# Kernel tuning notes

Hardware: AMD Instinct MI355X
Metric: run time of the kernel (lower is better)

Reference implementation:

```python
import jax, jax.numpy as jnp
import numpy as np
import math

D_MODEL = 1024
D_STATE = 64
DT_MIN = 0.001
DT_MAX = 0.1
BATCH = 4
SEQLEN = 4096


def make_hippo_matrix(N):
    P = np.sqrt(1 + 2 * np.arange(N))
    A = P[:, np.newaxis] * P[np.newaxis, :]
    A = np.tril(A) - np.diag(np.arange(N))
    return jnp.asarray(-A, dtype=jnp.float32)


def setup_inputs() -> dict:
    key = jax.random.key(0)
    k_u, k_B, k_C, k_D, k_dt = jax.random.split(key, 5)
    u = jax.random.normal(k_u, (BATCH, SEQLEN, D_MODEL), dtype=jnp.float32)
    A = make_hippo_matrix(D_STATE)  # (N, N) HiPPO-LegS buffer
    B = jax.random.normal(k_B, (D_STATE, 1), dtype=jnp.float32)
    C = jax.random.normal(k_C, (1, D_STATE), dtype=jnp.float32)
    D = jax.random.normal(k_D, (1,), dtype=jnp.float32)
    log_dt = (jax.random.uniform(k_dt, (1,), dtype=jnp.float32)
              * (math.log(DT_MAX) - math.log(DT_MIN)) + math.log(DT_MIN))
    return {"u": u, "A": A, "B": B, "C": C, "D": D, "log_dt": log_dt}


def _forward(u, A, B, C, D, log_dt):
    n = A.shape[0]
    dt = jnp.exp(log_dt)[0]
    A_bar = jax.scipy.linalg.expm(dt * A)                     # (N, N)
    B_bar = jnp.linalg.solve(A, (A_bar - jnp.eye(n, dtype=A.dtype)) @ B)  # (N, 1)
    bvec = B_bar[:, 0]          # (N,)
    cvec = C[0]                 # (N,)
    d_scalar = D[0]
    # Faithful to source: only channel 0 of u drives the SSM.
    u0 = u[:, :, 0]             # (Bn, L)

    def step(x, u_t):
        # x: (Bn, N), u_t: (Bn,)
        x = x @ A_bar.T + u_t[:, None] * bvec
        y = x @ cvec + d_scalar * u_t   # (Bn,)
        return x, y

    x0 = jnp.zeros((u.shape[0], n), dtype=u.dtype)
    _, ys = jax.lax.scan(step, x0, jnp.swapaxes(u0, 0, 1))   # (L, Bn)
    # Scalar output broadcast across all H channels (matches torch expand)
    y = jnp.broadcast_to(jnp.swapaxes(ys, 0, 1)[:, :, None], u.shape)
    return y


def reference(u, A, B, C, D, log_dt):
    return _forward(u, A, B, C, D, log_dt)
```

## Files before the change

kernel.cpp:

```cpp
#include <hip/hip_runtime.h>


#define NT 1024
#define MP 68
#define MSZ (64 * MP)
#define MOFF 4096
#define U0OFF (4096 + 8 * MSZ)

typedef __attribute__((ext_vector_type(8))) short v8s;
typedef __attribute__((ext_vector_type(4))) float v4f;

__device__ __forceinline__ unsigned short bf16r(float x) {
  union { float f; unsigned u; } v; v.f = x;
  unsigned r = v.u + 0x7fffu + ((v.u >> 16) & 1u);
  return (unsigned short)(r >> 16);
}
__device__ __forceinline__ float bf2f(unsigned short h) {
  union { unsigned u; float f; } v; v.u = ((unsigned)h) << 16;
  return v.f;
}

__device__ void mm_mfma(const float* gA, int aT, const float* gB, float* gC,
                        int pc, int nct, int colbase, unsigned short* FRAG) {
  const int t = threadIdx.x;
  __syncthreads();
  {
    const int slot = t >> 1;
    const int jh = (t & 1) * 4;
    const int l = slot & 63;
    const int Tq = slot >> 6;
    const int mrow = (Tq >> 1) * 16 + (l & 15);
    const int kk = (Tq & 1) * 32 + (l >> 4) * 8 + jh;
    float x0, x1, x2, x3;
    if (!aT) {
      const float4 f = *(const float4*)(gA + mrow * MP + kk);
      x0 = f.x; x1 = f.y; x2 = f.z; x3 = f.w;
    } else {
      x0 = gA[(kk + 0) * MP + mrow]; x1 = gA[(kk + 1) * MP + mrow];
      x2 = gA[(kk + 2) * MP + mrow]; x3 = gA[(kk + 3) * MP + mrow];
    }
    unsigned short h0 = bf16r(x0), h1 = bf16r(x1), h2 = bf16r(x2), h3 = bf16r(x3);
    ushort4 H, L;
    H.x = h0; H.y = h1; H.z = h2; H.w = h3;
    L.x = bf16r(x0 - bf2f(h0)); L.y = bf16r(x1 - bf2f(h1));
    L.z = bf16r(x2 - bf2f(h2)); L.w = bf16r(x3 - bf2f(h3));
    *(ushort4*)(FRAG + slot * 8 + jh) = H;
    *(ushort4*)(FRAG + 4096 + slot * 8 + jh) = L;
    const float y0 = gB[(kk + 0) * MP + mrow], y1 = gB[(kk + 1) * MP + mrow];
    const float y2 = gB[(kk + 2) * MP + mrow], y3 = gB[(kk + 3) * MP + mrow];
    unsigned short g0 = bf16r(y0), g1 = bf16r(y1), g2 = bf16r(y2), g3 = bf16r(y3);
    H.x = g0; H.y = g1; H.z = g2; H.w = g3;
    L.x = bf16r(y0 - bf2f(g0)); L.y = bf16r(y1 - bf2f(g1));
    L.z = bf16r(y2 - bf2f(g2)); L.w = bf16r(y3 - bf2f(g3));
    *(ushort4*)(FRAG + 8192 + slot * 8 + jh) = H;
    *(ushort4*)(FRAG + 12288 + slot * 8 + jh) = L;
  }
  __syncthreads();
  {
    const int w = t >> 6, l = t & 63;
    const int R = w >> 2, Cc = w & 3;
    if (Cc < nct) {
      const v8s Ah0 = *(const v8s*)(FRAG + ((R * 2 + 0) * 64 + l) * 8);
      const v8s Ah1 = *(const v8s*)(FRAG + ((R * 2 + 1) * 64 + l) * 8);
      const v8s Al0 = *(const v8s*)(FRAG + 4096 + ((R * 2 + 0) * 64 + l) * 8);
      const v8s Al1 = *(const v8s*)(FRAG + 4096 + ((R * 2 + 1) * 64 + l) * 8);
      const v8s Bh0 = *(const v8s*)(FRAG + 8192 + ((Cc * 2 + 0) * 64 + l) * 8);
      const v8s Bh1 = *(const v8s*)(FRAG + 8192 + ((Cc * 2 + 1) * 64 + l) * 8);
      const v8s Bl0 = *(const v8s*)(FRAG + 12288 + ((Cc * 2 + 0) * 64 + l) * 8);
      const v8s Bl1 = *(const v8s*)(FRAG + 12288 + ((Cc * 2 + 1) * 64 + l) * 8);
      v4f acc = {0.f, 0.f, 0.f, 0.f};
      acc = __builtin_amdgcn_mfma_f32_16x16x32_bf16(Ah0, Bh0, acc, 0, 0, 0);
      acc = __builtin_amdgcn_mfma_f32_16x16x32_bf16(Ah1, Bh1, acc, 0, 0, 0);
      acc = __builtin_amdgcn_mfma_f32_16x16x32_bf16(Ah0, Bl0, acc, 0, 0, 0);
      acc = __builtin_amdgcn_mfma_f32_16x16x32_bf16(Ah1, Bl1, acc, 0, 0, 0);
      acc = __builtin_amdgcn_mfma_f32_16x16x32_bf16(Al0, Bh0, acc, 0, 0, 0);
      acc = __builtin_amdgcn_mfma_f32_16x16x32_bf16(Al1, Bh1, acc, 0, 0, 0);
      const int col = colbase + Cc * 16 + (l & 15);
      const int r0 = R * 16 + (l >> 4) * 4;
      gC[(r0 + 0) * pc + col] = acc[0];
      gC[(r0 + 1) * pc + col] = acc[1];
      gC[(r0 + 2) * pc + col] = acc[2];
      gC[(r0 + 3) * pc + col] = acc[3];
    }
  }
  __syncthreads();
}

__device__ __forceinline__ void mv64(const float* Mm, const float* vin,
                                     float* vout, float* vscr) {
  __syncthreads();
  const int t = threadIdx.x, i = t & 63, c = t >> 6;
  const float4 m = *(const float4*)(Mm + i * MP + c * 4);
  vscr[t] = fmaf(m.x, vin[c * 4 + 0], fmaf(m.y, vin[c * 4 + 1],
            fmaf(m.z, vin[c * 4 + 2], m.w * vin[c * 4 + 3])));
  __syncthreads();
  if (t < 64) {
    float s = 0.f;
#pragma unroll
    for (int cc = 0; cc < 16; ++cc) s += vscr[cc * 64 + t];
    vout[t] = s;
  }
  __syncthreads();
}

__device__ void buildC(float* dst, const float* X, const float* X2, const float* X3,
                       float c0, float c1, float c2, float c3, int add) {
  __syncthreads();
  for (int e = threadIdx.x; e < 64 * MP; e += NT) {
    const int r = e / MP, c = e - r * MP;
    if (c < 64) {
      float v = c1 * X[e] + c2 * X2[e] + c3 * X3[e];
      if (c == r) v += c0;
      dst[e] = add ? dst[e] + v : v;
    }
  }
  __syncthreads();
}

__global__ __launch_bounds__(NT) void s4_setup(const float* __restrict__ u,
    const float* __restrict__ A, const float* __restrict__ Bv,
    const float* __restrict__ Cv, const float* __restrict__ logdt,
    float* __restrict__ ws) {
  if (blockIdx.x > 0) {
    const int idx = (blockIdx.x - 1) * NT + threadIdx.x;
    ws[U0OFF + idx] = u[(size_t)idx * 1024];
    return;
  }
  __shared__ __align__(16) unsigned short FRAG[16384];
  __shared__ float vscr[NT];
  __shared__ float va[64], vb[64], vg[64];
  __shared__ int s_s;
  float* Xc = (float*)FRAG;

  const int t = threadIdx.x;
  float* kbuf = ws;
  float* M0 = ws + MOFF;          float* M1 = M0 + MSZ;
  float* M2 = M1 + MSZ;           float* M3 = M2 + MSZ;
  float* M4 = M3 + MSZ;           float* M5 = M4 + MSZ;
  float* M6 = M5 + MSZ;           float* M7 = M6 + MSZ;
  const float dt = expf(logdt[0]);

  const float invf[17] = {1.f, 1.f, 1.f / 2.f, 1.f / 6.f, 1.f / 24.f, 1.f / 120.f,
                          1.f / 720.f, 1.f / 5040.f, 1.f / 40320.f, 1.f / 362880.f,
                          1.f / 3628800.f, 1.f / 39916800.f, 1.f / 479001600.f,
                          1.f / 6.2270208e9f, 1.f / 8.71782912e10f,
                          1.f / 1.307674368e12f, 1.f / 2.0922789888e13f};

  {
    const int j = t & 63, ch = t >> 6;
    float p = 0.f;
#pragma unroll
    for (int ii = 0; ii < 4; ++ii) p += fabsf(A[(ch * 4 + ii) * 64 + j]);
    vscr[t] = p;
    __syncthreads();
    if (t < 64) {
      float cs = 0.f;
#pragma unroll
      for (int c = 0; c < 16; ++c) cs += vscr[c * 64 + t];
      cs *= dt;
#pragma unroll
      for (int off = 32; off > 0; off >>= 1) cs = fmaxf(cs, __shfl_xor(cs, off));
      if (t == 0) {
        int s = 0;
        while (cs > 2.0f && s < 30) { cs *= 0.5f; ++s; }
        s_s = s;
      }
    }
    __syncthreads();
  }
  const int sq = s_s;
  const float scl = ldexpf(dt, -sq);

  {
    const float4 a4 = *(const float4*)(A + t * 4);
    float4 x;
    x.x = a4.x * scl; x.y = a4.y * scl; x.z = a4.z * scl; x.w = a4.w * scl;
    const int r = t >> 4, c4 = (t & 15) * 4;
    *(float4*)(M0 + r * MP + c4) = x;
    *(float4*)(Xc + r * MP + c4) = x;
  }
  __syncthreads();

  if (t < 64) { va[t] = Bv[t]; vg[t] = Bv[t]; }
  {
    float* vc = va; float* vn = vb;
    for (int k = 1; k <= 15; ++k) {
      mv64(Xc, vc, vn, vscr);
      if (t < 64) vg[t] = fmaf(vn[t], invf[k + 1], vg[t]);
      float* tmp = vc; vc = vn; vn = tmp;
    }
    __syncthreads();
  }

  mm_mfma(M0, 0, M0, M1, MP, 4, 0, FRAG);
  mm_mfma(M1, 0, M0, M2, MP, 4, 0, FRAG);
  mm_mfma(M1, 0, M1, M3, MP, 4, 0, FRAG);
  buildC(M5, M0, M1, M2, invf[12], invf[13], invf[14], invf[15], 0);
  mm_mfma(M5, 0, M3, M4, MP, 4, 0, FRAG);
  buildC(M4, M0, M1, M2, invf[8], invf[9], invf[10], invf[11], 1);
  mm_mfma(M4, 0, M3, M5, MP, 4, 0, FRAG);
  buildC(M5, M0, M1, M2, invf[4], invf[5], invf[6], invf[7], 1);
  mm_mfma(M5, 0, M3, M4, MP, 4, 0, FRAG);
  buildC(M4, M0, M1, M2, invf[0], invf[1], invf[2], invf[3], 1);

  float* F = M4; float* Fo = M5;
  for (int it = 0; it < sq; ++it) {
    mv64(F, vg, va, vscr);
    if (t < 64) vg[t] = 0.5f * (va[t] + vg[t]);
    mm_mfma(F, 0, F, Fo, MP, 4, 0, FRAG);
    float* tmp = F; F = Fo; Fo = tmp;
  }

  __syncthreads();
  {
    const int r = t >> 4, c4 = (t & 15) * 4;
    *(float4*)(Xc + r * MP + c4) = *(const float4*)(F + r * MP + c4);
  }
  if (t < 64) { va[t] = dt * vg[t]; M6[t * MP + 0] = dt * vg[t]; }
  __syncthreads();
  {
    float* vc = va; float* vn = vb;
    for (int r = 1; r < 16; ++r) {
      mv64(Xc, vc, vn, vscr);
      if (t < 64) M6[t * MP + r] = vn[t];
      float* tmp = vc; vc = vn; vn = tmp;
    }
    __syncthreads();
  }

  mm_mfma(F, 0, F, M0, MP, 4, 0, FRAG);
  mm_mfma(M0, 0, M0, M1, MP, 4, 0, FRAG);
  mm_mfma(M1, 0, M1, M0, MP, 4, 0, FRAG);
  mm_mfma(M0, 0, M0, M1, MP, 4, 0, FRAG);
  mm_mfma(M1, 0, M6, M6, MP, 1, 16, FRAG);
  mm_mfma(M1, 0, M1, M0, MP, 4, 0, FRAG);
  mm_mfma(M0, 0, M6, M6, MP, 2, 32, FRAG);
  mm_mfma(M0, 0, M0, M1, MP, 4, 0, FRAG);

  __syncthreads();
  for (int e = t; e < 4096; e += NT) {
    const int r = e >> 6, c = e & 63;
    Xc[c * MP + r] = M1[r * MP + c];
  }
  __syncthreads();
  if (t < 64) { va[t] = Cv[t]; M7[t * MP + 0] = Cv[t]; }
  __syncthreads();
  {
    float* vc = va; float* vn = vb;
    for (int q = 1; q < 16; ++q) {
      mv64(Xc, vc, vn, vscr);
      if (t < 64) M7[t * MP + q] = vn[t];
      float* tmp = vc; vc = vn; vn = tmp;
    }
    __syncthreads();
  }

  mm_mfma(M1, 0, M1, M0, MP, 4, 0, FRAG);
  mm_mfma(M0, 0, M0, M2, MP, 4, 0, FRAG);
  mm_mfma(M2, 0, M2, M0, MP, 4, 0, FRAG);
  mm_mfma(M0, 0, M0, M2, MP, 4, 0, FRAG);
  mm_mfma(M2, 1, M7, M7, MP, 1, 16, FRAG);
  mm_mfma(M2, 0, M2, M0, MP, 4, 0, FRAG);
  mm_mfma(M0, 1, M7, M7, MP, 2, 32, FRAG);

  mm_mfma(M7, 1, M6, kbuf, 64, 4, 0, FRAG);
}

__global__ __launch_bounds__(256) void s4_out(const float* __restrict__ ws,
                                              const float* __restrict__ Dp,
                                              float* __restrict__ out) {
  const int bid = blockIdx.x;
  const int b = bid >> 10;
  const int t0 = (bid & 1023) << 2;
  const float* kb = ws;
  const float* ub = ws + U0OFF + (b << 12);
  const int tid = threadIdx.x;
  const int t3 = t0 + 3;
  float a0 = 0.f, a1 = 0.f, a2 = 0.f, a3 = 0.f;
  for (int j = tid; j <= t3; j += 256) {
    const float kj = kb[j];
    if (j <= t0)     a0 = fmaf(kj, ub[t0 - j], a0);
    if (j <= t0 + 1) a1 = fmaf(kj, ub[t0 + 1 - j], a1);
    if (j <= t0 + 2) a2 = fmaf(kj, ub[t0 + 2 - j], a2);
    a3 = fmaf(kj, ub[t3 - j], a3);
  }
#pragma unroll
  for (int off = 32; off > 0; off >>= 1) {
    a0 += __shfl_xor(a0, off);
    a1 += __shfl_xor(a1, off);
    a2 += __shfl_xor(a2, off);
    a3 += __shfl_xor(a3, off);
  }
  __shared__ float red[4][4];
  __shared__ float sy[4];
  if ((tid & 63) == 0) {
    const int w = tid >> 6;
    red[0][w] = a0; red[1][w] = a1; red[2][w] = a2; red[3][w] = a3;
  }
  __syncthreads();
  if (tid < 4)
    sy[tid] = red[tid][0] + red[tid][1] + red[tid][2] + red[tid][3] +
              Dp[0] * ub[t0 + tid];
  __syncthreads();
  const int row = tid >> 6, l = tid & 63;
  const float y = sy[row];
  const float4 y4 = make_float4(y, y, y, y);
  float4* dst = (float4*)(out + ((size_t)(b << 12) + t0 + row) * 1024);
  dst[l] = y4; dst[l + 64] = y4; dst[l + 128] = y4; dst[l + 192] = y4;
}

extern "C" void kernel_launch(void* const* d_in, const int* in_sizes, int n_in,
                              void* d_out, int out_size, void* d_ws, size_t ws_size,
                              hipStream_t stream) {
  const float* u  = (const float*)d_in[0];
  const float* A  = (const float*)d_in[1];
  const float* B  = (const float*)d_in[2];
  const float* C  = (const float*)d_in[3];
  const float* D  = (const float*)d_in[4];
  const float* ld = (const float*)d_in[5];
  float* ws = (float*)d_ws;

  s4_setup<<<17, NT, 0, stream>>>(u, A, B, C, ld, ws);
  s4_out<<<4096, 256, 0, stream>>>(ws, D, (float*)d_out);
}
```

Measured before the change: 182.2 us.

## Keep running matrix power in LDS and restructure setup matrix chain

Restructures the single-block setup kernel so the running matrix (powers of A, expm result) lives in shared memory instead of global workspace. Matrix products are done in place through the fragment staging buffer, and the B-side Taylor series is evaluated with a Horner-style scheme on three precomputed powers. The Krylov/kernel blocks are stored transposed, so the final product needs no explicit transpose pass. The aim is to cut global-memory round trips and serial mat-vec steps in the latency-bound setup. The cost is heavier LDS use and in-place aliasing of the matrix operands.

```diff
diff --git a/kernel.cpp b/kernel.cpp
--- a/kernel.cpp
+++ b/kernel.cpp
@@ -3,9 +3,7 @@
 
 #define NT 1024
 #define MP 68
-#define MSZ (64 * MP)
-#define MOFF 4096
-#define U0OFF (4096 + 8 * MSZ)
+#define MB (64 * MP)
 
 typedef __attribute__((ext_vector_type(8))) short v8s;
 typedef __attribute__((ext_vector_type(4))) float v4f;
@@ -20,8 +18,10 @@
   return v.f;
 }
 
-__device__ void mm_mfma(const float* gA, int aT, const float* gB, float* gC,
-                        int pc, int nct, int colbase, unsigned short* FRAG) {
+__device__ void mm(const float* Ag, const float* Bs, int bT,
+                   float* Cd, int cpitch, float* Cd2,
+                   int nrt, int nct, int rowbase, int colbase,
+                   unsigned short* FRAG) {
   const int t = threadIdx.x;
   __syncthreads();
   {
@@ -31,66 +31,73 @@
     const int Tq = slot >> 6;
     const int mrow = (Tq >> 1) * 16 + (l & 15);
     const int kk = (Tq & 1) * 32 + (l >> 4) * 8 + jh;
-    float x0, x1, x2, x3;
-    if (!aT) {
-      const float4 f = *(const float4*)(gA + mrow * MP + kk);
-      x0 = f.x; x1 = f.y; x2 = f.z; x3 = f.w;
-    } else {
-      x0 = gA[(kk + 0) * MP + mrow]; x1 = gA[(kk + 1) * MP + mrow];
-      x2 = gA[(kk + 2) * MP + mrow]; x3 = gA[(kk + 3) * MP + mrow];
-    }
-    unsigned short h0 = bf16r(x0), h1 = bf16r(x1), h2 = bf16r(x2), h3 = bf16r(x3);
+    const float4 f = *(const float4*)(Ag + mrow * MP + kk);
     ushort4 H, L;
-    H.x = h0; H.y = h1; H.z = h2; H.w = h3;
-    L.x = bf16r(x0 - bf2f(h0)); L.y = bf16r(x1 - bf2f(h1));
-    L.z = bf16r(x2 - bf2f(h2)); L.w = bf16r(x3 - bf2f(h3));
+    unsigned short h;
+    h = bf16r(f.x); H.x = h; L.x = bf16r(f.x - bf2f(h));
+    h = bf16r(f.y); H.y = h; L.y = bf16r(f.y - bf2f(h));
+    h = bf16r(f.z); H.z = h; L.z = bf16r(f.z - bf2f(h));
+    h = bf16r(f.w); H.w = h; L.w = bf16r(f.w - bf2f(h));
     *(ushort4*)(FRAG + slot * 8 + jh) = H;
     *(ushort4*)(FRAG + 4096 + slot * 8 + jh) = L;
-    const float y0 = gB[(kk + 0) * MP + mrow], y1 = gB[(kk + 1) * MP + mrow];
-    const float y2 = gB[(kk + 2) * MP + mrow], y3 = gB[(kk + 3) * MP + mrow];
-    unsigned short g0 = bf16r(y0), g1 = bf16r(y1), g2 = bf16r(y2), g3 = bf16r(y3);
-    H.x = g0; H.y = g1; H.z = g2; H.w = g3;
-    L.x = bf16r(y0 - bf2f(g0)); L.y = bf16r(y1 - bf2f(g1));
-    L.z = bf16r(y2 - bf2f(g2)); L.w = bf16r(y3 - bf2f(g3));
+    float y0, y1, y2, y3;
+    if (bT) {
+      const float4 g = *(const float4*)(Bs + mrow * MP + kk);
+      y0 = g.x; y1 = g.y; y2 = g.z; y3 = g.w;
+    } else {
+      y0 = Bs[(kk + 0) * MP + mrow]; y1 = Bs[(kk + 1) * MP + mrow];
+      y2 = Bs[(kk + 2) * MP + mrow]; y3 = Bs[(kk + 3) * MP + mrow];
+    }
+    h = bf16r(y0); H.x = h; L.x = bf16r(y0 - bf2f(h));
+    h = bf16r(y1); H.y = h; L.y = bf16r(y1 - bf2f(h));
+    h = bf16r(y2); H.z = h; L.z = bf16r(y2 - bf2f(h));
+    h = bf16r(y3); H.w = h; L.w = bf16r(y3 - bf2f(h));
     *(ushort4*)(FRAG + 8192 + slot * 8 + jh) = H;
     *(ushort4*)(FRAG + 12288 + slot * 8 + jh) = L;
   }
   __syncthreads();
   {
     const int w = t >> 6, l = t & 63;
-    const int R = w >> 2, Cc = w & 3;
-    if (Cc < nct) {
-      const v8s Ah0 = *(const v8s*)(FRAG + ((R * 2 + 0) * 64 + l) * 8);
-      const v8s Ah1 = *(const v8s*)(FRAG + ((R * 2 + 1) * 64 + l) * 8);
-      const v8s Al0 = *(const v8s*)(FRAG + 4096 + ((R * 2 + 0) * 64 + l) * 8);
-      const v8s Al1 = *(const v8s*)(FRAG + 4096 + ((R * 2 + 1) * 64 + l) * 8);
-      const v8s Bh0 = *(const v8s*)(FRAG + 8192 + ((Cc * 2 + 0) * 64 + l) * 8);
-      const v8s Bh1 = *(const v8s*)(FRAG + 8192 + ((Cc * 2 + 1) * 64 + l) * 8);
-      const v8s Bl0 = *(const v8s*)(FRAG + 12288 + ((Cc * 2 + 0) * 64 + l) * 8);
-      const v8s Bl1 = *(const v8s*)(FRAG + 12288 + ((Cc * 2 + 1) * 64 + l) * 8);
-      v4f acc = {0.f, 0.f, 0.f, 0.f};
-      acc = __builtin_amdgcn_mfma_f32_16x16x32_bf16(Ah0, Bh0, acc, 0, 0, 0);
-      acc = __builtin_amdgcn_mfma_f32_16x16x32_bf16(Ah1, Bh1, acc, 0, 0, 0);
-      acc = __builtin_amdgcn_mfma_f32_16x16x32_bf16(Ah0, Bl0, acc, 0, 0, 0);
-      acc = __builtin_amdgcn_mfma_f32_16x16x32_bf16(Ah1, Bl1, acc, 0, 0, 0);
-      acc = __builtin_amdgcn_mfma_f32_16x16x32_bf16(Al0, Bh0, acc, 0, 0, 0);
-      acc = __builtin_amdgcn_mfma_f32_16x16x32_bf16(Al1, Bh1, acc, 0, 0, 0);
-      const int col = colbase + Cc * 16 + (l & 15);
-      const int r0 = R * 16 + (l >> 4) * 4;
-      gC[(r0 + 0) * pc + col] = acc[0];
-      gC[(r0 + 1) * pc + col] = acc[1];
-      gC[(r0 + 2) * pc + col] = acc[2];
-      gC[(r0 + 3) * pc + col] = acc[3];
-    }
-  }
-  __syncthreads();
-}
-
-__device__ __forceinline__ void mv64(const float* Mm, const float* vin,
-                                     float* vout, float* vscr) {
+    if (w < 4 && w < nrt) {
+      const v8s Ah0 = *(const v8s*)(FRAG + ((w * 2 + 0) * 64 + l) * 8);
+      const v8s Ah1 = *(const v8s*)(FRAG + ((w * 2 + 1) * 64 + l) * 8);
+      const v8s Al0 = *(const v8s*)(FRAG + 4096 + ((w * 2 + 0) * 64 + l) * 8);
+      const v8s Al1 = *(const v8s*)(FRAG + 4096 + ((w * 2 + 1) * 64 + l) * 8);
+      for (int Cc = 0; Cc < nct; ++Cc) {
+        const v8s Bh0 = *(const v8s*)(FRAG + 8192 + ((Cc * 2 + 0) * 64 + l) * 8);
+        const v8s Bh1 = *(const v8s*)(FRAG + 8192 + ((Cc * 2 + 1) * 64 + l) * 8);
+        const v8s Bl0 = *(const v8s*)(FRAG + 12288 + ((Cc * 2 + 0) * 64 + l) * 8);
+        const v8s Bl1 = *(const v8s*)(FRAG + 12288 + ((Cc * 2 + 1) * 64 + l) * 8);
+        v4f acc = {0.f, 0.f, 0.f, 0.f};
+        acc = __builtin_amdgcn_mfma_f32_16x16x32_bf16(Ah0, Bh0, acc, 0, 0, 0);
+        acc = __builtin_amdgcn_mfma_f32_16x16x32_bf16(Ah1, Bh1, acc, 0, 0, 0);
+        acc = __builtin_amdgcn_mfma_f32_16x16x32_bf16(Ah0, Bl0, acc, 0, 0, 0);
+        acc = __builtin_amdgcn_mfma_f32_16x16x32_bf16(Ah1, Bl1, acc, 0, 0, 0);
+        acc = __builtin_amdgcn_mfma_f32_16x16x32_bf16(Al0, Bh0, acc, 0, 0, 0);
+        acc = __builtin_amdgcn_mfma_f32_16x16x32_bf16(Al1, Bh1, acc, 0, 0, 0);
+        const int col = colbase + Cc * 16 + (l & 15);
+        const int r0 = rowbase + w * 16 + (l >> 4) * 4;
+        Cd[(r0 + 0) * cpitch + col] = acc[0];
+        Cd[(r0 + 1) * cpitch + col] = acc[1];
+        Cd[(r0 + 2) * cpitch + col] = acc[2];
+        Cd[(r0 + 3) * cpitch + col] = acc[3];
+        if (Cd2) {
+          Cd2[(r0 + 0) * MP + col] = acc[0];
+          Cd2[(r0 + 1) * MP + col] = acc[1];
+          Cd2[(r0 + 2) * MP + col] = acc[2];
+          Cd2[(r0 + 3) * MP + col] = acc[3];
+        }
+      }
+    }
+  }
+  __syncthreads();
+}
+
+__device__ __forceinline__ void mv64row(const float* M, const float* vin,
+                                        float* vout, float* vscr) {
   __syncthreads();
   const int t = threadIdx.x, i = t & 63, c = t >> 6;
-  const float4 m = *(const float4*)(Mm + i * MP + c * 4);
+  const float4 m = *(const float4*)(M + i * MP + c * 4);
   vscr[t] = fmaf(m.x, vin[c * 4 + 0], fmaf(m.y, vin[c * 4 + 1],
             fmaf(m.z, vin[c * 4 + 2], m.w * vin[c * 4 + 3])));
   __syncthreads();
@@ -103,15 +110,34 @@
   __syncthreads();
 }
 
-__device__ void buildC(float* dst, const float* X, const float* X2, const float* X3,
-                       float c0, float c1, float c2, float c3, int add) {
-  __syncthreads();
-  for (int e = threadIdx.x; e < 64 * MP; e += NT) {
+__device__ __forceinline__ void mv64colT(const float* M, const float* vin,
+                                         float* vout, float* vscr) {
+  __syncthreads();
+  const int t = threadIdx.x, i = t & 63, c = t >> 6;
+  float p = 0.f;
+#pragma unroll
+  for (int j = 0; j < 4; ++j) p = fmaf(M[(c * 4 + j) * MP + i], vin[c * 4 + j], p);
+  vscr[t] = p;
+  __syncthreads();
+  if (t < 64) {
+    float s = 0.f;
+#pragma unroll
+    for (int cc = 0; cc < 16; ++cc) s += vscr[cc * 64 + t];
+    vout[t] = s;
+  }
+  __syncthreads();
+}
+
+__device__ void buildG(float* dst, const float* X, const float* X2, const float* X3,
+                       float c0, float c1, float c2, float c3, const float* addsrc) {
+  __syncthreads();
+  for (int e = threadIdx.x; e < MB; e += NT) {
     const int r = e / MP, c = e - r * MP;
     if (c < 64) {
       float v = c1 * X[e] + c2 * X2[e] + c3 * X3[e];
-      if (c == r) v += c0;
-      dst[e] = add ? dst[e] + v : v;
+      if (r == c) v += c0;
+      if (addsrc) v += addsrc[e];
+      dst[e] = v;
     }
   }
   __syncthreads();
@@ -123,21 +149,24 @@
     float* __restrict__ ws) {
   if (blockIdx.x > 0) {
     const int idx = (blockIdx.x - 1) * NT + threadIdx.x;
-    ws[U0OFF + idx] = u[(size_t)idx * 1024];
+    ws[4096 + idx] = u[(size_t)idx * 1024];
     return;
   }
+  __shared__ __align__(16) float S0[MB];
   __shared__ __align__(16) unsigned short FRAG[16384];
-  __shared__ float vscr[NT];
-  __shared__ float va[64], vb[64], vg[64];
+  __shared__ float vB[64], v1[64], v2[64], v3[64], va[64], vb[64], vg[64];
   __shared__ int s_s;
-  float* Xc = (float*)FRAG;
+  float* vscr = (float*)FRAG;
 
   const int t = threadIdx.x;
   float* kbuf = ws;
-  float* M0 = ws + MOFF;          float* M1 = M0 + MSZ;
-  float* M2 = M1 + MSZ;           float* M3 = M2 + MSZ;
-  float* M4 = M3 + MSZ;           float* M5 = M4 + MSZ;
-  float* M6 = M5 + MSZ;           float* M7 = M6 + MSZ;
+  float* gX   = ws + 20480;
+  float* gX2  = ws + 24832;
+  float* gX3  = ws + 29184;
+  float* gU0  = ws + 33536;
+  float* gU1  = ws + 37888;
+  float* gBRT = ws + 42240;
+  float* gCQT = ws + 46592;
   const float dt = expf(logdt[0]);
 
   const float invf[17] = {1.f, 1.f, 1.f / 2.f, 1.f / 6.f, 1.f / 24.f, 1.f / 120.f,
@@ -176,94 +205,84 @@
     float4 x;
     x.x = a4.x * scl; x.y = a4.y * scl; x.z = a4.z * scl; x.w = a4.w * scl;
     const int r = t >> 4, c4 = (t & 15) * 4;
-    *(float4*)(M0 + r * MP + c4) = x;
-    *(float4*)(Xc + r * MP + c4) = x;
-  }
-  __syncthreads();
-
-  if (t < 64) { va[t] = Bv[t]; vg[t] = Bv[t]; }
-  {
-    float* vc = va; float* vn = vb;
-    for (int k = 1; k <= 15; ++k) {
-      mv64(Xc, vc, vn, vscr);
-      if (t < 64) vg[t] = fmaf(vn[t], invf[k + 1], vg[t]);
-      float* tmp = vc; vc = vn; vn = tmp;
-    }
-    __syncthreads();
-  }
-
-  mm_mfma(M0, 0, M0, M1, MP, 4, 0, FRAG);
-  mm_mfma(M1, 0, M0, M2, MP, 4, 0, FRAG);
-  mm_mfma(M1, 0, M1, M3, MP, 4, 0, FRAG);
-  buildC(M5, M0, M1, M2, invf[12], invf[13], invf[14], invf[15], 0);
-  mm_mfma(M5, 0, M3, M4, MP, 4, 0, FRAG);
-  buildC(M4, M0, M1, M2, invf[8], invf[9], invf[10], invf[11], 1);
-  mm_mfma(M4, 0, M3, M5, MP, 4, 0, FRAG);
-  buildC(M5, M0, M1, M2, invf[4], invf[5], invf[6], invf[7], 1);
-  mm_mfma(M5, 0, M3, M4, MP, 4, 0, FRAG);
-  buildC(M4, M0, M1, M2, invf[0], invf[1], invf[2], invf[3], 1);
-
-  float* F = M4; float* Fo = M5;
+    *(float4*)(S0 + r * MP + c4) = x;
+    *(float4*)(gX + r * MP + c4) = x;
+  }
+  if (t < 64) vB[t] = Bv[t];
+
+  mm(S0, S0, 0, S0, MP, gX2, 4, 4, 0, 0, FRAG);
+  mm(gX, S0, 0, gX3, MP, nullptr, 4, 4, 0, 0, FRAG);
+  mm(S0, S0, 0, S0, MP, nullptr, 4, 4, 0, 0, FRAG);
+
+  mv64row(gX,  vB, v1, vscr);
+  mv64row(gX2, vB, v2, vscr);
+  mv64row(gX3, vB, v3, vscr);
+  if (t < 64)
+    va[t] = invf[13] * vB[t] + invf[14] * v1[t] + invf[15] * v2[t] + invf[16] * v3[t];
+  mv64row(S0, va, vb, vscr);
+  if (t < 64)
+    va[t] = invf[9] * vB[t] + invf[10] * v1[t] + invf[11] * v2[t] + invf[12] * v3[t] + vb[t];
+  mv64row(S0, va, vb, vscr);
+  if (t < 64)
+    va[t] = invf[5] * vB[t] + invf[6] * v1[t] + invf[7] * v2[t] + invf[8] * v3[t] + vb[t];
+  mv64row(S0, va, vb, vscr);
+  if (t < 64)
+    vg[t] = invf[1] * vB[t] + invf[2] * v1[t] + invf[3] * v2[t] + invf[4] * v3[t] + vb[t];
+
+  buildG(gU0, gX, gX2, gX3, invf[12], invf[13], invf[14], invf[15], nullptr);
+  mm(gU0, S0, 0, gU1, MP, nullptr, 4, 4, 0, 0, FRAG);
+  buildG(gU1, gX, gX2, gX3, invf[8], invf[9], invf[10], invf[11], gU1);
+  mm(gU1, S0, 0, gU0, MP, nullptr, 4, 4, 0, 0, FRAG);
+  buildG(gU0, gX, gX2, gX3, invf[4], invf[5], invf[6], invf[7], gU0);
+  mm(gU0, S0, 0, S0, MP, nullptr, 4, 4, 0, 0, FRAG);
+  buildG(S0, gX, gX2, gX3, invf[0], invf[1], invf[2], invf[3], S0);
+
   for (int it = 0; it < sq; ++it) {
-    mv64(F, vg, va, vscr);
+    mv64row(S0, vg, va, vscr);
     if (t < 64) vg[t] = 0.5f * (va[t] + vg[t]);
-    mm_mfma(F, 0, F, Fo, MP, 4, 0, FRAG);
-    float* tmp = F; F = Fo; Fo = tmp;
-  }
-
-  __syncthreads();
-  {
-    const int r = t >> 4, c4 = (t & 15) * 4;
-    *(float4*)(Xc + r * MP + c4) = *(const float4*)(F + r * MP + c4);
-  }
-  if (t < 64) { va[t] = dt * vg[t]; M6[t * MP + 0] = dt * vg[t]; }
-  __syncthreads();
+    mm(S0, S0, 0, S0, MP, nullptr, 4, 4, 0, 0, FRAG);
+  }
+
+  __syncthreads();
+  if (t < 64) { va[t] = dt * vg[t]; gBRT[t] = dt * vg[t]; }
   {
     float* vc = va; float* vn = vb;
     for (int r = 1; r < 16; ++r) {
-      mv64(Xc, vc, vn, vscr);
-      if (t < 64) M6[t * MP + r] = vn[t];
+      mv64row(S0, vc, vn, vscr);
+      if (t < 64) gBRT[r * MP + t] = vn[t];
       float* tmp = vc; vc = vn; vn = tmp;
     }
-    __syncthreads();
-  }
-
-  mm_mfma(F, 0, F, M0, MP, 4, 0, FRAG);
-  mm_mfma(M0, 0, M0, M1, MP, 4, 0, FRAG);
-  mm_mfma(M1, 0, M1, M0, MP, 4, 0, FRAG);
-  mm_mfma(M0, 0, M0, M1, MP, 4, 0, FRAG);
-  mm_mfma(M1, 0, M6, M6, MP, 1, 16, FRAG);
-  mm_mfma(M1, 0, M1, M0, MP, 4, 0, FRAG);
-  mm_mfma(M0, 0, M6, M6, MP, 2, 32, FRAG);
-  mm_mfma(M0, 0, M0, M1, MP, 4, 0, FRAG);
-
-  __syncthreads();
-  for (int e = t; e < 4096; e += NT) {
-    const int r = e >> 6, c = e & 63;
-    Xc[c * MP + r] = M1[r * MP + c];
-  }
-  __syncthreads();
-  if (t < 64) { va[t] = Cv[t]; M7[t * MP + 0] = Cv[t]; }
-  __syncthreads();
+  }
+
+  mm(S0, S0, 0, S0, MP, nullptr, 4, 4, 0, 0, FRAG);
+  mm(S0, S0, 0, S0, MP, nullptr, 4, 4, 0, 0, FRAG);
+  mm(S0, S0, 0, S0, MP, nullptr, 4, 4, 0, 0, FRAG);
+  mm(S0, S0, 0, S0, MP, nullptr, 4, 4, 0, 0, FRAG);
+  mm(gBRT, S0, 1, gBRT, MP, nullptr, 1, 4, 16, 0, FRAG);
+  mm(S0, S0, 0, S0, MP, nullptr, 4, 4, 0, 0, FRAG);
+  mm(gBRT, S0, 1, gBRT, MP, nullptr, 2, 4, 32, 0, FRAG);
+  mm(S0, S0, 0, S0, MP, nullptr, 4, 4, 0, 0, FRAG);
+
+  __syncthreads();
+  if (t < 64) { va[t] = Cv[t]; gCQT[t] = Cv[t]; }
   {
     float* vc = va; float* vn = vb;
-    for (int q = 1; q < 16; ++q) {
-      mv64(Xc, vc, vn, vscr);
-      if (t < 64) M7[t * MP + q] = vn[t];
+    for (int qx = 1; qx < 16; ++qx) {
+      mv64colT(S0, vc, vn, vscr);
+      if (t < 64) gCQT[qx * MP + t] = vn[t];
       float* tmp = vc; vc = vn; vn = tmp;
     }
-    __syncthreads();
-  }
-
-  mm_mfma(M1, 0, M1, M0, MP, 4, 0, FRAG);
-  mm_mfma(M0, 0, M0, M2, MP, 4, 0, FRAG);
-  mm_mfma(M2, 0, M2, M0, MP, 4, 0, FRAG);
-  mm_mfma(M0, 0, M0, M2, MP, 4, 0, FRAG);
-  mm_mfma(M2, 1, M7, M7, MP, 1, 16, FRAG);
-  mm_mfma(M2, 0, M2, M0, MP, 4, 0, FRAG);
-  mm_mfma(M0, 1, M7, M7, MP, 2, 32, FRAG);
-
-  mm_mfma(M7, 1, M6, kbuf, 64, 4, 0, FRAG);
+  }
+
+  mm(S0, S0, 0, S0, MP, nullptr, 4, 4, 0, 0, FRAG);
+  mm(S0, S0, 0, S0, MP, nullptr, 4, 4, 0, 0, FRAG);
+  mm(S0, S0, 0, S0, MP, nullptr, 4, 4, 0, 0, FRAG);
+  mm(S0, S0, 0, S0, MP, nullptr, 4, 4, 0, 0, FRAG);
+  mm(gCQT, S0, 0, gCQT, MP, nullptr, 1, 4, 16, 0, FRAG);
+  mm(S0, S0, 0, S0, MP, nullptr, 4, 4, 0, 0, FRAG);
+  mm(gCQT, S0, 0, gCQT, MP, nullptr, 2, 4, 32, 0, FRAG);
+
+  mm(gCQT, gBRT, 1, kbuf, 64, nullptr, 4, 4, 0, 0, FRAG);
 }
 
 __global__ __launch_bounds__(256) void s4_out(const float* __restrict__ ws,
@@ -273,7 +292,7 @@
   const int b = bid >> 10;
   const int t0 = (bid & 1023) << 2;
   const float* kb = ws;
-  const float* ub = ws + U0OFF + (b << 12);
+  const float* ub = ws + 4096 + (b << 12);
   const int tid = threadIdx.x;
   const int t3 = t0 + 3;
   float a0 = 0.f, a1 = 0.f, a2 = 0.f, a3 = 0.f;
```

Result: faster. 169.0 us (-7.3%).
